# Performance work log

Hardware: AMD Instinct MI355X
Metric: run time of the kernel (lower is better)

The kernel has to match this reference:

```python
import jax, jax.numpy as jnp
import numpy as np

OUT_DIM = 64
NUM_HEADS = 8
HID = NUM_HEADS * OUT_DIM  # 512
ALPHA = 0.01  # leaky relu slope
N_NODES = 20000
N_EDGES = 100000
MP_LEN = 3


def setup_inputs() -> dict:
    key = jax.random.key(0)
    ks = jax.random.split(key, 8)
    s = 1.0 / np.sqrt(HID)
    return {
        "features": jax.random.normal(ks[0], (N_NODES, OUT_DIM), jnp.float32),
        "W_ih": jax.random.normal(ks[1], (3 * HID, OUT_DIM), jnp.float32) * s,
        "W_hh": jax.random.normal(ks[2], (3 * HID, HID), jnp.float32) * s,
        "b_ih": jax.random.normal(ks[3], (3 * HID,), jnp.float32) * s,
        "b_hh": jax.random.normal(ks[4], (3 * HID,), jnp.float32) * s,
        "attn": jax.random.normal(ks[5], (NUM_HEADS, OUT_DIM), jnp.float32) * 0.1,
        "edge_metapath_indices": jax.random.randint(ks[6], (N_EDGES, MP_LEN), 0, N_NODES),
        "edge_dst": jax.random.randint(ks[7], (N_EDGES,), 0, N_NODES),
    }


def _gru_last_hidden(x_seq, W_ih, W_hh, b_ih, b_hh):
    """x_seq: [L, E, D] -> final hidden [E, HID] (torch nn.GRU math, h0=0)."""
    E = x_seq.shape[1]
    h0 = jnp.zeros((E, HID), x_seq.dtype)

    def step(h, x):
        gi = x @ W_ih.T + b_ih  # [E, 3*HID]
        gh = h @ W_hh.T + b_hh  # [E, 3*HID]
        i_r, i_z, i_n = jnp.split(gi, 3, axis=-1)
        h_r, h_z, h_n = jnp.split(gh, 3, axis=-1)
        r = jax.nn.sigmoid(i_r + h_r)
        z = jax.nn.sigmoid(i_z + h_z)
        n = jnp.tanh(i_n + r * h_n)
        h_new = (1.0 - z) * n + z * h
        return h_new, None

    h_last, _ = jax.lax.scan(step, h0, x_seq)
    return h_last


def reference(features, W_ih, W_hh, b_ih, b_hh, attn,
              edge_metapath_indices, edge_dst):
    N = features.shape[0]
    # gather metapath node features: [E, L, D] -> GRU over L
    edata = features[edge_metapath_indices]
    h = _gru_last_hidden(jnp.transpose(edata, (1, 0, 2)), W_ih, W_hh, b_ih, b_hh)
    eft = h.reshape(-1, NUM_HEADS, OUT_DIM)  # [E, H, D]
    # attention logits per edge/head + leaky relu
    a = jnp.sum(eft * attn[None], axis=-1)  # [E, H]
    a = jnp.where(a >= 0, a, ALPHA * a)
    # edge softmax grouped by destination node
    amax = jax.ops.segment_max(a, edge_dst, num_segments=N)  # [N, H]
    ea = jnp.exp(a - amax[edge_dst])
    denom = jax.ops.segment_sum(ea, edge_dst, num_segments=N)  # [N, H]
    alpha = ea / denom[edge_dst]  # [E, H]
    # weighted message aggregation (sum) to destination nodes
    msg = eft * alpha[:, :, None]  # [E, H, D]
    ret = jax.ops.segment_sum(msg, edge_dst, num_segments=N)  # [N, H, D]
    return ret
```

## Files before the change

### kernel.cpp

```cpp
#include <hip/hip_runtime.h>
#include <hip/hip_bf16.h>

#define N_NODES 20000
#define N_EDGES 100000
#define HID 512
#define G3 1536
#define NH 8
#define OD 64

typedef __hip_bfloat16 bf16;
typedef __attribute__((ext_vector_type(8))) short bf16x8;
typedef __attribute__((ext_vector_type(4))) float f32x4;

__device__ __forceinline__ float frcp(float x) { return __builtin_amdgcn_rcpf(x); }
__device__ __forceinline__ float fsig(float x) { return frcp(1.0f + __expf(-x)); }
__device__ __forceinline__ float ftanh(float x) { return 1.0f - 2.0f * frcp(__expf(2.0f * x) + 1.0f); }
__device__ __forceinline__ float b2f(bf16 b) { return __bfloat162float(b); }
__device__ __forceinline__ bf16 f2b(float f) { return __float2bfloat16(f); }
__device__ __forceinline__ float bs2f(short s) {
    return __uint_as_float(((unsigned)(unsigned short)s) << 16);
}
__device__ __forceinline__ float us2f(unsigned short s) {
    return __uint_as_float(((unsigned)s) << 16);
}
__device__ __forceinline__ short f2bs(float f) {
    bf16 b = __float2bfloat16(f);
    return *reinterpret_cast<short*>(&b);
}
__device__ __forceinline__ unsigned ford(float f) {
    unsigned u = __float_as_uint(f);
    return (u & 0x80000000u) ? ~u : (u | 0x80000000u);
}
__device__ __forceinline__ float iford(unsigned u) {
    return __uint_as_float((u & 0x80000000u) ? (u & 0x7fffffffu) : ~u);
}

__device__ __forceinline__ void g2l16(const void* g, void* l) {
#if __has_builtin(__builtin_amdgcn_global_load_lds)
    __builtin_amdgcn_global_load_lds((const __attribute__((address_space(1))) char*)g,
                                     (__attribute__((address_space(3))) char*)l, 16, 0, 0);
#else
    *(bf16x8*)l = *(const bf16x8*)g;
#endif
}


__global__ __launch_bounds__(256) void k_prep(const float* __restrict__ Whh,
                                              const float* __restrict__ Wih,
                                              bf16* __restrict__ WTs,
                                              float* __restrict__ WIT) {
    int t = blockIdx.x * 256 + threadIdx.x;
    if (t < 98304) {
        int T = t >> 10, c = (t >> 6) & 15, l = t & 63;
        int n = T * 16 + (l & 15);
        int k = c * 32 + ((l >> 4) << 3);
        const float* src = Whh + (size_t)n * 512 + k;
        bf16x8 v;
#pragma unroll
        for (int j = 0; j < 8; ++j) v[j] = f2bs(src[j]);
        *(bf16x8*)(WTs + (size_t)t * 8) = v;
    } else {
        int u = t - 98304;
        int d = u / 1536, j = u % 1536;
        WIT[u] = Wih[(size_t)j * 64 + d];
    }
}

__global__ __launch_bounds__(256) void k_count(const int* __restrict__ dst,
                                               unsigned* __restrict__ cnt) {
    int e = blockIdx.x * 256 + threadIdx.x;
    if (e < N_EDGES) atomicAdd(&cnt[dst[e]], 1u);
}

#define SCAN_CH 79
__global__ __launch_bounds__(256) void k_scan(const unsigned* __restrict__ cnt,
                                              unsigned* __restrict__ base,
                                              unsigned* __restrict__ cursor) {
    __shared__ unsigned ls[256];
    int t = threadIdx.x;
    int s0 = t * SCAN_CH;
    int s1 = s0 + SCAN_CH < N_NODES ? s0 + SCAN_CH : N_NODES;
    unsigned s = 0;
    for (int i = s0; i < s1; ++i) s += cnt[i];
    ls[t] = s;
    __syncthreads();
    for (int d = 1; d < 256; d <<= 1) {
        unsigned v = (t >= d) ? ls[t - d] : 0u;
        __syncthreads();
        ls[t] += v;
        __syncthreads();
    }
    unsigned run = ls[t] - s;
    for (int i = s0; i < s1; ++i) {
        base[i] = run; cursor[i] = run; run += cnt[i];
    }
    if (t == 255) base[N_NODES] = ls[255];
}

__global__ __launch_bounds__(256) void k_fill(const int* __restrict__ dst,
                                              unsigned* __restrict__ cursor,
                                              unsigned* __restrict__ csr) {
    int e = blockIdx.x * 256 + threadIdx.x;
    if (e < N_EDGES) {
        unsigned p = atomicAdd(&cursor[dst[e]], 1u);
        csr[p] = (unsigned)e;
    }
}

__global__ __launch_bounds__(256) void k_gi(const float* __restrict__ feat,
                                            const float* __restrict__ WIT,
                                            const float* __restrict__ b_ih,
                                            const float* __restrict__ b_hh,
                                            bf16* __restrict__ G,
                                            bf16* __restrict__ H1) {
    __shared__ float fs[16][64];
    const int n0 = blockIdx.x * 16;
    const int k = blockIdx.y * 256 + threadIdx.x;
    for (int i = threadIdx.x; i < 16 * 64; i += 256)
        fs[0][i] = feat[(size_t)n0 * 64 + i];
    __syncthreads();
    float acc[3][16];
#pragma unroll
    for (int g = 0; g < 3; ++g) {
        float b = b_ih[g * 512 + k];
#pragma unroll
        for (int e = 0; e < 16; ++e) acc[g][e] = b;
    }
    for (int d = 0; d < 64; d += 4) {
        float w[3][4];
#pragma unroll
        for (int u = 0; u < 4; ++u)
#pragma unroll
            for (int g = 0; g < 3; ++g)
                w[g][u] = WIT[(size_t)(d + u) * G3 + g * 512 + k];
#pragma unroll
        for (int e = 0; e < 16; ++e) {
            float4 f = *(const float4*)&fs[e][d];
#pragma unroll
            for (int g = 0; g < 3; ++g)
                acc[g][e] += w[g][0] * f.x + w[g][1] * f.y + w[g][2] * f.z + w[g][3] * f.w;
        }
    }
    const float br = b_hh[k], bz = b_hh[512 + k], bn = b_hh[1024 + k];
#pragma unroll
    for (int e = 0; e < 16; ++e) {
        bf16* dst = G + (size_t)(n0 + e) * G3 + k * 3;
        dst[0] = f2b(acc[0][e]);
        dst[1] = f2b(acc[1][e]);
        dst[2] = f2b(acc[2][e]);
        float r1 = fsig(acc[0][e] + br);
        float z1 = fsig(acc[1][e] + bz);
        float n1 = ftanh(acc[2][e] + r1 * bn);
        H1[(size_t)(n0 + e) * HID + k] = f2b((1.0f - z1) * n1);
    }
}

__global__ __launch_bounds__(256, 2) void k_gh2(const bf16* __restrict__ H1,
                                                const bf16* __restrict__ WTs,
                                                const float* __restrict__ b_hh,
                                                bf16* __restrict__ GH2) {
    __shared__ short Bs[3 * 8192];
    const int tid = threadIdx.x;
    const int wave = tid >> 6, lane = tid & 63;
    const int m0 = blockIdx.x * 128;
    const int k0 = (lane >> 4) << 3;

    bf16x8 afrag[2][16];
#pragma unroll
    for (int t = 0; t < 2; ++t) {
        int row = m0 + wave * 32 + t * 16 + (lane & 15);
        int ar = row < N_NODES ? row : N_NODES - 1;
#pragma unroll
        for (int c = 0; c < 16; ++c)
            afrag[t][c] = *(const bf16x8*)(H1 + (size_t)ar * HID + c * 32 + k0);
    }

    const bf16* wp[12];
    short* lp[12];
#pragma unroll
    for (int i = 0; i < 12; ++i) {
        int p = tid + i * 256;
        int g = p >> 10, q = p & 1023;
        wp[i] = WTs + (size_t)g * 32 * 8192 + q * 8;
        lp[i] = &Bs[g * 8192 + q * 8];
    }

    const int col = lane & 15;
    const int qb = (lane >> 4) << 2;
    for (int jt = 0; jt < 32; ++jt) {
        __syncthreads();
#pragma unroll
        for (int i = 0; i < 12; ++i) {
            g2l16(wp[i], lp[i]);
            wp[i] += 8192;
        }
        __syncthreads();
        f32x4 acc[2][3];
#pragma unroll
        for (int t = 0; t < 2; ++t)
#pragma unroll
            for (int g = 0; g < 3; ++g) acc[t][g] = (f32x4){0, 0, 0, 0};
        const int boff = lane * 8;
#pragma unroll
        for (int c = 0; c < 16; ++c) {
            bf16x8 b0 = *(const bf16x8*)&Bs[0 * 8192 + c * 512 + boff];
            bf16x8 b1 = *(const bf16x8*)&Bs[1 * 8192 + c * 512 + boff];
            bf16x8 b2 = *(const bf16x8*)&Bs[2 * 8192 + c * 512 + boff];
#pragma unroll
            for (int t = 0; t < 2; ++t) {
                acc[t][0] = __builtin_amdgcn_mfma_f32_16x16x32_bf16(afrag[t][c], b0, acc[t][0], 0, 0, 0);
                acc[t][1] = __builtin_amdgcn_mfma_f32_16x16x32_bf16(afrag[t][c], b1, acc[t][1], 0, 0, 0);
                acc[t][2] = __builtin_amdgcn_mfma_f32_16x16x32_bf16(afrag[t][c], b2, acc[t][2], 0, 0, 0);
            }
        }
        const int cj = jt * 16 + col;
        const float br = b_hh[cj], bz = b_hh[512 + cj], bn = b_hh[1024 + cj];
#pragma unroll
        for (int t = 0; t < 2; ++t)
#pragma unroll
            for (int q = 0; q < 4; ++q) {
                int e = m0 + wave * 32 + t * 16 + qb + q;
                if (e < N_NODES) {
                    bf16* dst = GH2 + (size_t)e * G3 + cj * 3;
                    dst[0] = f2b(acc[t][0][q] + br);
                    dst[1] = f2b(acc[t][1][q] + bz);
                    dst[2] = f2b(acc[t][2][q] + bn);
                }
            }
    }
}

__global__ __launch_bounds__(256) void k_h2(const bf16* __restrict__ G,
                                            const bf16* __restrict__ GH2,
                                            const bf16* __restrict__ H1,
                                            const int* __restrict__ emi,
                                            bf16* __restrict__ h2) {
    size_t i = (size_t)blockIdx.x * 256 + threadIdx.x;
    int e = (int)(i >> 6);
    int kc = (int)(i & 63) * 8;
    int i0 = emi[(size_t)e * 3 + 0];
    int i1 = emi[(size_t)e * 3 + 1];
    const bf16* g1p = G + (size_t)i1 * G3 + kc * 3;
    const bf16* ghp = GH2 + (size_t)i0 * G3 + kc * 3;
    bf16x8 h1v = *(const bf16x8*)(H1 + (size_t)i0 * HID + kc);
    short s1[24], sh[24];
    {
        bf16x8 a0 = *(const bf16x8*)g1p, a1 = *(const bf16x8*)(g1p + 8), a2 = *(const bf16x8*)(g1p + 16);
        bf16x8 c0 = *(const bf16x8*)ghp, c1 = *(const bf16x8*)(ghp + 8), c2 = *(const bf16x8*)(ghp + 16);
#pragma unroll
        for (int j = 0; j < 8; ++j) {
            s1[j] = a0[j]; s1[8 + j] = a1[j]; s1[16 + j] = a2[j];
            sh[j] = c0[j]; sh[8 + j] = c1[j]; sh[16 + j] = c2[j];
        }
    }
    bf16x8 out;
#pragma unroll
    for (int j = 0; j < 8; ++j) {
        float r = fsig(bs2f(s1[j * 3 + 0]) + bs2f(sh[j * 3 + 0]));
        float z = fsig(bs2f(s1[j * 3 + 1]) + bs2f(sh[j * 3 + 1]));
        float n = ftanh(bs2f(s1[j * 3 + 2]) + r * bs2f(sh[j * 3 + 2]));
        out[j] = f2bs((1.0f - z) * n + z * bs2f(h1v[j]));
    }
    *(bf16x8*)(h2 + (size_t)e * HID + kc) = out;
}

__global__ __launch_bounds__(256) void k_gemm3(const bf16* __restrict__ G,
                                               const bf16* __restrict__ WTs,
                                               const float* __restrict__ b_hh,
                                               const int* __restrict__ emi,
                                               bf16* __restrict__ h2) {
    __shared__ short Bs[3 * 8192];
    __shared__ int si2[64];
    const int tid = threadIdx.x;
    const int wave = tid >> 6, lane = tid & 63;
    const int m0 = blockIdx.x * 64;
    if (tid < 64) {
        int e = m0 + tid;
        si2[tid] = emi[(size_t)(e < N_EDGES ? e : N_EDGES - 1) * 3 + 2];
    }
    const int k0 = (lane >> 4) << 3;

    bf16x8 afrag[16];
    {
        int row = m0 + wave * 16 + (lane & 15);
        int ar = row < N_EDGES ? row : N_EDGES - 1;
#pragma unroll
        for (int c = 0; c < 16; ++c)
            afrag[c] = *(const bf16x8*)(h2 + (size_t)ar * HID + c * 32 + k0);
    }

    const bf16* wp[12];
    short* lp[12];
#pragma unroll
    for (int i = 0; i < 12; ++i) {
        int p = tid + i * 256;
        int g = p >> 10, q = p & 1023;
        wp[i] = WTs + (size_t)g * 32 * 8192 + q * 8;
        lp[i] = &Bs[g * 8192 + q * 8];
    }

    const int col = lane & 15;
    const int qb = (lane >> 4) << 2;
    for (int jt = 0; jt < 32; ++jt) {
        __syncthreads();
#pragma unroll
        for (int i = 0; i < 12; ++i) {
            g2l16(wp[i], lp[i]);
            wp[i] += 8192;
        }
        const int cj = jt * 16 + col;
        const float br = b_hh[cj], bz = b_hh[512 + cj], bn = b_hh[1024 + cj];
        unsigned short pg[4][3], ph[4];
#pragma unroll
        for (int q = 0; q < 4; ++q) {
            int li = wave * 16 + qb + q;
            int e = m0 + li;
            int ec = e < N_EDGES ? e : N_EDGES - 1;
            const unsigned short* g2p =
                (const unsigned short*)(G + (size_t)si2[li] * G3 + cj * 3);
            pg[q][0] = g2p[0]; pg[q][1] = g2p[1]; pg[q][2] = g2p[2];
            ph[q] = ((const unsigned short*)h2)[(size_t)ec * HID + cj];
        }
        __syncthreads();
        f32x4 a0 = {0, 0, 0, 0}, a1 = {0, 0, 0, 0}, a2 = {0, 0, 0, 0};
        const int boff = lane * 8;
#pragma unroll
        for (int c = 0; c < 16; ++c) {
            bf16x8 b0 = *(const bf16x8*)&Bs[0 * 8192 + c * 512 + boff];
            bf16x8 b1 = *(const bf16x8*)&Bs[1 * 8192 + c * 512 + boff];
            bf16x8 b2 = *(const bf16x8*)&Bs[2 * 8192 + c * 512 + boff];
            a0 = __builtin_amdgcn_mfma_f32_16x16x32_bf16(afrag[c], b0, a0, 0, 0, 0);
            a1 = __builtin_amdgcn_mfma_f32_16x16x32_bf16(afrag[c], b1, a1, 0, 0, 0);
            a2 = __builtin_amdgcn_mfma_f32_16x16x32_bf16(afrag[c], b2, a2, 0, 0, 0);
        }
#pragma unroll
        for (int q = 0; q < 4; ++q) {
            int e = m0 + wave * 16 + qb + q;
            if (e < N_EDGES) {
                float r = fsig(us2f(pg[q][0]) + a0[q] + br);
                float z = fsig(us2f(pg[q][1]) + a1[q] + bz);
                float ng = ftanh(us2f(pg[q][2]) + r * (a2[q] + bn));
                h2[(size_t)e * HID + cj] = f2b((1.0f - z) * ng + z * us2f(ph[q]));
            }
        }
    }
}

__global__ __launch_bounds__(256) void k_logits(const bf16* __restrict__ eft,
                                                const float* __restrict__ attn,
                                                const int* __restrict__ dst,
                                                float* __restrict__ a,
                                                unsigned* __restrict__ amax) {
    int i = blockIdx.x * 256 + threadIdx.x;
    int e = i >> 3, h = i & 7;
    const __hip_bfloat162* f2 = (const __hip_bfloat162*)(eft + (size_t)e * HID + h * OD);
    const float* at = attn + h * OD;
    float s = 0.f;
#pragma unroll
    for (int d = 0; d < OD / 2; ++d) {
        float2 fv = __bfloat1622float2(f2[d]);
        s += fv.x * at[2 * d] + fv.y * at[2 * d + 1];
    }
    s = (s >= 0.f) ? s : 0.01f * s;
    a[i] = s;
    atomicMax(&amax[(size_t)dst[e] * NH + h], ford(s));
}

__global__ __launch_bounds__(256) void k_ea(const int* __restrict__ dst,
                                            const unsigned* __restrict__ amax,
                                            float* __restrict__ a,
                                            float* __restrict__ denom) {
    int i = blockIdx.x * 256 + threadIdx.x;
    int e = i >> 3, h = i & 7;
    float m = iford(amax[(size_t)dst[e] * NH + h]);
    float v = __expf(a[i] - m);
    a[i] = v;
    atomicAdd(&denom[(size_t)dst[e] * NH + h], v);
}

__global__ __launch_bounds__(256) void k_out(const bf16* __restrict__ eft,
                                             const float* __restrict__ a,
                                             const float* __restrict__ denom,
                                             const unsigned* __restrict__ base,
                                             const unsigned* __restrict__ csr,
                                             float* __restrict__ out) {
    int n = blockIdx.x;
    int k = blockIdx.y * 256 + threadIdx.x;
    int h = k >> 6;
    unsigned b0 = base[n], b1 = base[n + 1];
    float rden = (b1 > b0) ? frcp(denom[(size_t)n * NH + h]) : 0.0f;
    float acc = 0.f;
    for (unsigned i = b0; i < b1; ++i) {
        unsigned e = csr[i];
        float al = a[(size_t)e * NH + h];
        acc += b2f(eft[(size_t)e * HID + k]) * al;
    }
    out[(size_t)n * HID + k] = acc * rden;
}

extern "C" void kernel_launch(void* const* d_in, const int* in_sizes, int n_in,
                              void* d_out, int out_size, void* d_ws, size_t ws_size,
                              hipStream_t stream) {
    (void)in_sizes; (void)n_in; (void)ws_size; (void)out_size;
    const float* feat = (const float*)d_in[0];
    const float* W_ih = (const float*)d_in[1];
    const float* W_hh = (const float*)d_in[2];
    const float* b_ih = (const float*)d_in[3];
    const float* b_hh = (const float*)d_in[4];
    const float* attn = (const float*)d_in[5];
    const int* emi = (const int*)d_in[6];
    const int* dst = (const int*)d_in[7];
    float* out = (float*)d_out;

    char* ws = (char*)d_ws;
    bf16* G = (bf16*)ws;
    bf16* GH2 = (bf16*)(ws + 61440000);
    bf16* h2 = (bf16*)(ws + 122880000);
    bf16* WTs = (bf16*)(ws + 225280000);
    float* WIT = (float*)(ws + 226852864);
    float* a = (float*)(ws + 227246080);
    unsigned* amax = (unsigned*)(ws + 230446080);
    float* denom = (float*)(ws + 231086080);
    unsigned* cnt = (unsigned*)(ws + 231726080);
    unsigned* base = (unsigned*)(ws + 231806080);
    unsigned* cursor = (unsigned*)(ws + 231886088);
    unsigned* csr = (unsigned*)(ws + 231966088);
    bf16* H1 = (bf16*)(ws + 232366088);

    (void)hipMemsetAsync(amax, 0, 1360000, stream);

    k_prep<<<768, 256, 0, stream>>>(W_hh, W_ih, WTs, WIT);
    k_count<<<391, 256, 0, stream>>>(dst, cnt);
    k_scan<<<1, 256, 0, stream>>>(cnt, base, cursor);
    k_fill<<<391, 256, 0, stream>>>(dst, cursor, csr);
    k_gi<<<dim3(1250, 2), 256, 0, stream>>>(feat, WIT, b_ih, b_hh, G, H1);
    k_gh2<<<157, 256, 0, stream>>>(H1, WTs, b_hh, GH2);
    k_h2<<<25000, 256, 0, stream>>>(G, GH2, H1, emi, h2);
    k_gemm3<<<1563, 256, 0, stream>>>(G, WTs, b_hh, emi, h2);
    k_logits<<<3125, 256, 0, stream>>>(h2, attn, dst, a, amax);
    k_ea<<<3125, 256, 0, stream>>>(dst, amax, a, denom);
    k_out<<<dim3(N_NODES, 2), 256, 0, stream>>>(h2, a, denom, base, csr, out);
}
```

Before: 798.8 us.

## Double-buffer weight tiles per gate in GRU GEMMs to overlap loads with MFMA

Both GRU hidden-state GEMM kernels now stage one 16 KB gate slice of W_hh at a time into a two-slot LDS ring and prefetch the next slice while MFMAs run on the current one. This replaces the old load-all-three-gates-then-compute pattern, which had two barriers per tile and no overlap. Shared memory per block drops from 48 KB to 32 KB, launch bounds rise to 4 blocks, and k_gh2 shrinks to 64 rows per block with twice as many blocks. The cost is three barriers per column tile instead of two, and k_gh2 reuses each weight tile over fewer rows.

```diff
diff --git a/kernel.cpp b/kernel.cpp
--- a/kernel.cpp
+++ b/kernel.cpp
@@ -155,78 +155,98 @@
     }
 }
 
-__global__ __launch_bounds__(256, 2) void k_gh2(const bf16* __restrict__ H1,
+__global__ __launch_bounds__(256, 4) void k_gh2(const bf16* __restrict__ H1,
                                                 const bf16* __restrict__ WTs,
                                                 const float* __restrict__ b_hh,
                                                 bf16* __restrict__ GH2) {
-    __shared__ short Bs[3 * 8192];
+    __shared__ short Bs[2][8192];
     const int tid = threadIdx.x;
     const int wave = tid >> 6, lane = tid & 63;
-    const int m0 = blockIdx.x * 128;
+    const int m0 = blockIdx.x * 64;
     const int k0 = (lane >> 4) << 3;
 
-    bf16x8 afrag[2][16];
-#pragma unroll
-    for (int t = 0; t < 2; ++t) {
-        int row = m0 + wave * 32 + t * 16 + (lane & 15);
+    bf16x8 afrag[16];
+    {
+        int row = m0 + wave * 16 + (lane & 15);
         int ar = row < N_NODES ? row : N_NODES - 1;
 #pragma unroll
         for (int c = 0; c < 16; ++c)
-            afrag[t][c] = *(const bf16x8*)(H1 + (size_t)ar * HID + c * 32 + k0);
-    }
-
-    const bf16* wp[12];
-    short* lp[12];
-#pragma unroll
-    for (int i = 0; i < 12; ++i) {
-        int p = tid + i * 256;
-        int g = p >> 10, q = p & 1023;
-        wp[i] = WTs + (size_t)g * 32 * 8192 + q * 8;
-        lp[i] = &Bs[g * 8192 + q * 8];
+            afrag[c] = *(const bf16x8*)(H1 + (size_t)ar * HID + c * 32 + k0);
     }
 
     const int col = lane & 15;
     const int qb = (lane >> 4) << 2;
+    const int boff = lane * 8;
+
+#pragma unroll
+    for (int i = 0; i < 4; ++i) {
+        int q = tid + i * 256;
+        g2l16(WTs + (size_t)q * 8, &Bs[0][q * 8]);
+    }
+    __syncthreads();
+
+    int cur = 0;
     for (int jt = 0; jt < 32; ++jt) {
-        __syncthreads();
-#pragma unroll
-        for (int i = 0; i < 12; ++i) {
-            g2l16(wp[i], lp[i]);
-            wp[i] += 8192;
-        }
-        __syncthreads();
-        f32x4 acc[2][3];
-#pragma unroll
-        for (int t = 0; t < 2; ++t)
-#pragma unroll
-            for (int g = 0; g < 3; ++g) acc[t][g] = (f32x4){0, 0, 0, 0};
-        const int boff = lane * 8;
-#pragma unroll
-        for (int c = 0; c < 16; ++c) {
-            bf16x8 b0 = *(const bf16x8*)&Bs[0 * 8192 + c * 512 + boff];
-            bf16x8 b1 = *(const bf16x8*)&Bs[1 * 8192 + c * 512 + boff];
-            bf16x8 b2 = *(const bf16x8*)&Bs[2 * 8192 + c * 512 + boff];
-#pragma unroll
-            for (int t = 0; t < 2; ++t) {
-                acc[t][0] = __builtin_amdgcn_mfma_f32_16x16x32_bf16(afrag[t][c], b0, acc[t][0], 0, 0, 0);
-                acc[t][1] = __builtin_amdgcn_mfma_f32_16x16x32_bf16(afrag[t][c], b1, acc[t][1], 0, 0, 0);
-                acc[t][2] = __builtin_amdgcn_mfma_f32_16x16x32_bf16(afrag[t][c], b2, acc[t][2], 0, 0, 0);
-            }
-        }
         const int cj = jt * 16 + col;
+        f32x4 a0 = {0, 0, 0, 0}, a1 = {0, 0, 0, 0}, a2 = {0, 0, 0, 0};
         const float br = b_hh[cj], bz = b_hh[512 + cj], bn = b_hh[1024 + cj];
-#pragma unroll
-        for (int t = 0; t < 2; ++t)
+        {
+#pragma unroll
+            for (int i = 0; i < 4; ++i) {
+                int q = tid + i * 256;
+                g2l16(WTs + 262144 + (size_t)jt * 8192 + q * 8, &Bs[cur ^ 1][q * 8]);
+            }
+            const short* cb = &Bs[cur][0];
+#pragma unroll
+            for (int c = 0; c < 16; ++c) {
+                bf16x8 b = *(const bf16x8*)&cb[c * 512 + boff];
+                a0 = __builtin_amdgcn_mfma_f32_16x16x32_bf16(afrag[c], b, a0, 0, 0, 0);
+            }
+            __syncthreads();
+            cur ^= 1;
+        }
+        {
+#pragma unroll
+            for (int i = 0; i < 4; ++i) {
+                int q = tid + i * 256;
+                g2l16(WTs + 524288 + (size_t)jt * 8192 + q * 8, &Bs[cur ^ 1][q * 8]);
+            }
+            const short* cb = &Bs[cur][0];
+#pragma unroll
+            for (int c = 0; c < 16; ++c) {
+                bf16x8 b = *(const bf16x8*)&cb[c * 512 + boff];
+                a1 = __builtin_amdgcn_mfma_f32_16x16x32_bf16(afrag[c], b, a1, 0, 0, 0);
+            }
+            __syncthreads();
+            cur ^= 1;
+        }
+        {
+            if (jt < 31) {
+#pragma unroll
+                for (int i = 0; i < 4; ++i) {
+                    int q = tid + i * 256;
+                    g2l16(WTs + (size_t)(jt + 1) * 8192 + q * 8, &Bs[cur ^ 1][q * 8]);
+                }
+            }
+            const short* cb = &Bs[cur][0];
+#pragma unroll
+            for (int c = 0; c < 16; ++c) {
+                bf16x8 b = *(const bf16x8*)&cb[c * 512 + boff];
+                a2 = __builtin_amdgcn_mfma_f32_16x16x32_bf16(afrag[c], b, a2, 0, 0, 0);
+            }
 #pragma unroll
             for (int q = 0; q < 4; ++q) {
-                int e = m0 + wave * 32 + t * 16 + qb + q;
+                int e = m0 + wave * 16 + qb + q;
                 if (e < N_NODES) {
                     bf16* dst = GH2 + (size_t)e * G3 + cj * 3;
-                    dst[0] = f2b(acc[t][0][q] + br);
-                    dst[1] = f2b(acc[t][1][q] + bz);
-                    dst[2] = f2b(acc[t][2][q] + bn);
+                    dst[0] = f2b(a0[q] + br);
+                    dst[1] = f2b(a1[q] + bz);
+                    dst[2] = f2b(a2[q] + bn);
                 }
             }
+            __syncthreads();
+            cur ^= 1;
+        }
     }
 }
 
@@ -264,12 +284,12 @@
     *(bf16x8*)(h2 + (size_t)e * HID + kc) = out;
 }
 
-__global__ __launch_bounds__(256) void k_gemm3(const bf16* __restrict__ G,
-                                               const bf16* __restrict__ WTs,
-                                               const float* __restrict__ b_hh,
-                                               const int* __restrict__ emi,
-                                               bf16* __restrict__ h2) {
-    __shared__ short Bs[3 * 8192];
+__global__ __launch_bounds__(256, 4) void k_gemm3(const bf16* __restrict__ G,
+                                                  const bf16* __restrict__ WTs,
+                                                  const float* __restrict__ b_hh,
+                                                  const int* __restrict__ emi,
+                                                  bf16* __restrict__ h2) {
+    __shared__ short Bs[2][8192];
     __shared__ int si2[64];
     const int tid = threadIdx.x;
     const int wave = tid >> 6, lane = tid & 63;
@@ -289,59 +309,90 @@
             afrag[c] = *(const bf16x8*)(h2 + (size_t)ar * HID + c * 32 + k0);
     }
 
-    const bf16* wp[12];
-    short* lp[12];
-#pragma unroll
-    for (int i = 0; i < 12; ++i) {
-        int p = tid + i * 256;
-        int g = p >> 10, q = p & 1023;
-        wp[i] = WTs + (size_t)g * 32 * 8192 + q * 8;
-        lp[i] = &Bs[g * 8192 + q * 8];
-    }
-
     const int col = lane & 15;
     const int qb = (lane >> 4) << 2;
+    const int boff = lane * 8;
+
+#pragma unroll
+    for (int i = 0; i < 4; ++i) {
+        int q = tid + i * 256;
+        g2l16(WTs + (size_t)q * 8, &Bs[0][q * 8]);
+    }
+    __syncthreads();
+
+    int cur = 0;
     for (int jt = 0; jt < 32; ++jt) {
-        __syncthreads();
-#pragma unroll
-        for (int i = 0; i < 12; ++i) {
-            g2l16(wp[i], lp[i]);
-            wp[i] += 8192;
-        }
         const int cj = jt * 16 + col;
-        const float br = b_hh[cj], bz = b_hh[512 + cj], bn = b_hh[1024 + cj];
+        f32x4 a0 = {0, 0, 0, 0}, a1 = {0, 0, 0, 0}, a2 = {0, 0, 0, 0};
+        float br, bz, bn;
         unsigned short pg[4][3], ph[4];
-#pragma unroll
-        for (int q = 0; q < 4; ++q) {
-            int li = wave * 16 + qb + q;
-            int e = m0 + li;
-            int ec = e < N_EDGES ? e : N_EDGES - 1;
-            const unsigned short* g2p =
-                (const unsigned short*)(G + (size_t)si2[li] * G3 + cj * 3);
-            pg[q][0] = g2p[0]; pg[q][1] = g2p[1]; pg[q][2] = g2p[2];
-            ph[q] = ((const unsigned short*)h2)[(size_t)ec * HID + cj];
-        }
-        __syncthreads();
-        f32x4 a0 = {0, 0, 0, 0}, a1 = {0, 0, 0, 0}, a2 = {0, 0, 0, 0};
-        const int boff = lane * 8;
-#pragma unroll
-        for (int c = 0; c < 16; ++c) {
-            bf16x8 b0 = *(const bf16x8*)&Bs[0 * 8192 + c * 512 + boff];
-            bf16x8 b1 = *(const bf16x8*)&Bs[1 * 8192 + c * 512 + boff];
-            bf16x8 b2 = *(const bf16x8*)&Bs[2 * 8192 + c * 512 + boff];
-            a0 = __builtin_amdgcn_mfma_f32_16x16x32_bf16(afrag[c], b0, a0, 0, 0, 0);
-            a1 = __builtin_amdgcn_mfma_f32_16x16x32_bf16(afrag[c], b1, a1, 0, 0, 0);
-            a2 = __builtin_amdgcn_mfma_f32_16x16x32_bf16(afrag[c], b2, a2, 0, 0, 0);
-        }
-#pragma unroll
-        for (int q = 0; q < 4; ++q) {
-            int e = m0 + wave * 16 + qb + q;
-            if (e < N_EDGES) {
-                float r = fsig(us2f(pg[q][0]) + a0[q] + br);
-                float z = fsig(us2f(pg[q][1]) + a1[q] + bz);
-                float ng = ftanh(us2f(pg[q][2]) + r * (a2[q] + bn));
-                h2[(size_t)e * HID + cj] = f2b((1.0f - z) * ng + z * us2f(ph[q]));
-            }
+        {
+            br = b_hh[cj]; bz = b_hh[512 + cj]; bn = b_hh[1024 + cj];
+#pragma unroll
+            for (int q = 0; q < 4; ++q) {
+                int li = wave * 16 + qb + q;
+                int e = m0 + li;
+                int ec = e < N_EDGES ? e : N_EDGES - 1;
+                const unsigned short* g2p =
+                    (const unsigned short*)(G + (size_t)si2[li] * G3 + cj * 3);
+                pg[q][0] = g2p[0]; pg[q][1] = g2p[1]; pg[q][2] = g2p[2];
+                ph[q] = ((const unsigned short*)h2)[(size_t)ec * HID + cj];
+            }
+#pragma unroll
+            for (int i = 0; i < 4; ++i) {
+                int q = tid + i * 256;
+                g2l16(WTs + 262144 + (size_t)jt * 8192 + q * 8, &Bs[cur ^ 1][q * 8]);
+            }
+            const short* cb = &Bs[cur][0];
+#pragma unroll
+            for (int c = 0; c < 16; ++c) {
+                bf16x8 b = *(const bf16x8*)&cb[c * 512 + boff];
+                a0 = __builtin_amdgcn_mfma_f32_16x16x32_bf16(afrag[c], b, a0, 0, 0, 0);
+            }
+            __syncthreads();
+            cur ^= 1;
+        }
+        {
+#pragma unroll
+            for (int i = 0; i < 4; ++i) {
+                int q = tid + i * 256;
+                g2l16(WTs + 524288 + (size_t)jt * 8192 + q * 8, &Bs[cur ^ 1][q * 8]);
+            }
+            const short* cb = &Bs[cur][0];
+#pragma unroll
+            for (int c = 0; c < 16; ++c) {
+                bf16x8 b = *(const bf16x8*)&cb[c * 512 + boff];
+                a1 = __builtin_amdgcn_mfma_f32_16x16x32_bf16(afrag[c], b, a1, 0, 0, 0);
+            }
+            __syncthreads();
+            cur ^= 1;
+        }
+        {
+            if (jt < 31) {
+#pragma unroll
+                for (int i = 0; i < 4; ++i) {
+                    int q = tid + i * 256;
+                    g2l16(WTs + (size_t)(jt + 1) * 8192 + q * 8, &Bs[cur ^ 1][q * 8]);
+                }
+            }
+            const short* cb = &Bs[cur][0];
+#pragma unroll
+            for (int c = 0; c < 16; ++c) {
+                bf16x8 b = *(const bf16x8*)&cb[c * 512 + boff];
+                a2 = __builtin_amdgcn_mfma_f32_16x16x32_bf16(afrag[c], b, a2, 0, 0, 0);
+            }
+#pragma unroll
+            for (int q = 0; q < 4; ++q) {
+                int e = m0 + wave * 16 + qb + q;
+                if (e < N_EDGES) {
+                    float r = fsig(us2f(pg[q][0]) + a0[q] + br);
+                    float z = fsig(us2f(pg[q][1]) + a1[q] + bz);
+                    float ng = ftanh(us2f(pg[q][2]) + r * (a2[q] + bn));
+                    h2[(size_t)e * HID + cj] = f2b((1.0f - z) * ng + z * us2f(ph[q]));
+                }
+            }
+            __syncthreads();
+            cur ^= 1;
         }
     }
 }
@@ -434,7 +485,7 @@
     k_scan<<<1, 256, 0, stream>>>(cnt, base, cursor);
     k_fill<<<391, 256, 0, stream>>>(dst, cursor, csr);
     k_gi<<<dim3(1250, 2), 256, 0, stream>>>(feat, WIT, b_ih, b_hh, G, H1);
-    k_gh2<<<157, 256, 0, stream>>>(H1, WTs, b_hh, GH2);
+    k_gh2<<<313, 256, 0, stream>>>(H1, WTs, b_hh, GH2);
     k_h2<<<25000, 256, 0, stream>>>(G, GH2, H1, emi, h2);
     k_gemm3<<<1563, 256, 0, stream>>>(G, WTs, b_hh, emi, h2);
     k_logits<<<3125, 256, 0, stream>>>(h2, attn, dst, a, amax);
```

Measured after the change: 764.9 us. 1.04x faster.
